# Kernel optimization log

Hardware: AMD Instinct MI355X
Metric: run time of the kernel (lower is better)

The kernel has to match this reference:

```python
import jax, jax.numpy as jnp
import numpy as np

B, S, I, H, O = 64, 512, 256, 1024, 128

def setup_inputs() -> dict:
    key = jax.random.key(0)
    ks = jax.random.split(key, 9)
    s_in = 1.0 / np.sqrt(I)
    s_h = 1.0 / np.sqrt(H)
    return {
        "x": jax.random.normal(ks[0], (B, S, I), dtype=jnp.float32),
        "W_in": jax.random.uniform(ks[1], (H, I), jnp.float32, -s_in, s_in),
        "b_in": jax.random.uniform(ks[2], (H,), jnp.float32, -s_in, s_in),
        "W_rec": jax.random.uniform(ks[3], (H, H), jnp.float32, -s_h, s_h),
        "b_rec": jax.random.uniform(ks[4], (H,), jnp.float32, -s_h, s_h),
        "tau_m": jnp.full((H,), 2.0, dtype=jnp.float32),
        "tau_n": jnp.full((H,), 2.0, dtype=jnp.float32),
        "W_out": jax.random.uniform(ks[5], (O, H), jnp.float32, -s_h, s_h),
        "b_out": jax.random.uniform(ks[6], (O,), jnp.float32, -s_h, s_h),
    }

def reference(x, W_in, b_in, W_rec, b_rec, tau_m, tau_n, W_out, b_out):
    b, s, _ = x.shape
    h = W_in.shape[0]
    alpha = jax.nn.sigmoid(tau_m)  # [H]
    beta = jax.nn.sigmoid(tau_n)   # [H]
    # Precompute feedforward GEMM for all timesteps at once: [B,S,H]
    ff = jnp.einsum('bsi,hi->bsh', x, W_in) + b_in

    def step(carry, ff_t):
        mem, d, prev_spike = carry  # each [B,H]
        total = ff_t + prev_spike @ W_rec.T + b_rec
        d = beta * d + (1.0 - beta) * total
        mem = alpha * mem + (1.0 - alpha) * d
        spike = (mem > 1.0).astype(mem.dtype)
        mem = mem * (1.0 - spike)
        out = jax.nn.sigmoid(spike @ W_out.T + b_out)  # [B,O]
        return (mem, d, spike), out

    zeros = jnp.zeros((b, h), dtype=x.dtype)
    _, outs = jax.lax.scan(step, (zeros, zeros, zeros), jnp.swapaxes(ff, 0, 1))
    return jnp.swapaxes(outs, 0, 1)  # [B,S,O]
```

## Files before the change

kernel.cpp:

```cpp
#include <hip/hip_runtime.h>
#include <hip/hip_bf16.h>
#include <stdint.h>

#define B_ 64
#define S_ 512
#define I_ 256
#define H_ 1024
#define O_ 128
#define M_ (B_*S_)

typedef float f32x4 __attribute__((ext_vector_type(4)));
typedef unsigned short u16x4 __attribute__((ext_vector_type(4)));
typedef unsigned short u16x8 __attribute__((ext_vector_type(8)));

__device__ __forceinline__ unsigned short f2bf(float f) {
    unsigned u = __float_as_uint(f);
    u += 0x7FFFu + ((u >> 16) & 1u);
    return (unsigned short)(u >> 16);
}
__device__ __forceinline__ float bf2f(unsigned short s) {
    return __uint_as_float((unsigned)s << 16);
}

__global__ void __launch_bounds__(256) k0_convert(
    const float* __restrict__ x, const float* __restrict__ Win,
    uint8_t* __restrict__ xf8, uint8_t* __restrict__ wf8,
    unsigned* __restrict__ firstCross, unsigned* __restrict__ cnt)
{
    const unsigned tid = blockIdx.x * 256 + threadIdx.x;
    const float* src;
    uint8_t* dst;
    if (tid < 524288u) {
        unsigned T = tid >> 11, rem = tid & 2047;
        unsigned kt = rem >> 10, g = (rem >> 7) & 7, r = rem & 127;
        src = x + ((size_t)(T * 128 + r)) * 256 + kt * 128 + g * 16;
        dst = xf8 + (size_t)tid * 16;
    } else {
        unsigned t2 = tid - 524288u;
        unsigned T = t2 >> 11, rem = t2 & 2047;
        unsigned kt = rem >> 10, g = (rem >> 7) & 7, r = rem & 127;
        src = Win + ((size_t)(T * 128 + r)) * 256 + kt * 128 + g * 16;
        dst = wf8 + (size_t)t2 * 16;
    }
    const float4* s4 = (const float4*)src;
    float4 a = s4[0], b = s4[1], c = s4[2], e = s4[3];
    int w0 = 0, w1 = 0, w2 = 0, w3 = 0;
    w0 = __builtin_amdgcn_cvt_pk_fp8_f32(a.x, a.y, w0, false);
    w0 = __builtin_amdgcn_cvt_pk_fp8_f32(a.z, a.w, w0, true);
    w1 = __builtin_amdgcn_cvt_pk_fp8_f32(b.x, b.y, w1, false);
    w1 = __builtin_amdgcn_cvt_pk_fp8_f32(b.z, b.w, w1, true);
    w2 = __builtin_amdgcn_cvt_pk_fp8_f32(c.x, c.y, w2, false);
    w2 = __builtin_amdgcn_cvt_pk_fp8_f32(c.z, c.w, w2, true);
    w3 = __builtin_amdgcn_cvt_pk_fp8_f32(e.x, e.y, w3, false);
    w3 = __builtin_amdgcn_cvt_pk_fp8_f32(e.z, e.w, w3, true);
    int4 o; o.x = w0; o.y = w1; o.z = w2; o.w = w3;
    *(int4*)dst = o;
    if (blockIdx.x == 0) {
        if (threadIdx.x < 64) firstCross[threadIdx.x] = 0xFFFFFFFFu;
        else if (threadIdx.x < 128) cnt[threadIdx.x - 64] = 0u;
    }
}

__global__ void __launch_bounds__(256) kf_gemm_scan(
    const uint8_t* __restrict__ xf8, const uint8_t* __restrict__ wf8,
    const float* __restrict__ b_in, const float* __restrict__ b_rec,
    const float* __restrict__ tau_m, const float* __restrict__ tau_n,
    const float* __restrict__ b_out,
    unsigned* __restrict__ firstCross, unsigned* __restrict__ cnt,
    float* __restrict__ out)
{
    __shared__ uint8_t lsbuf[32768];
    __shared__ int lastFlag;
    uint8_t* lA = lsbuf;
    uint8_t* lB = lsbuf + 16384;

    const int tid  = threadIdx.x;
    const int w    = tid >> 6;
    const int lane = tid & 63;
    const int idx  = blockIdx.x;
    const int b    = (idx & 7) | ((idx >> 6) << 3);
    const int hn   = (idx >> 3) & 7;
    const int wave_m = (w >> 1) * 64;
    const int wave_n = (w & 1) * 64;
    const int colrow = lane & 15;
    const int quad   = lane >> 4;

    float alpha = 0.f, beta = 0.f, cbr = 0.f, oma = 0.f, ombr = 0.f;
    float d = 0.f, mem = 0.f;
    unsigned cross = 0xFFFFFFFFu;
    if (tid < 128) {
        const int hs = hn * 128 + tid;
        alpha = 1.f / (1.f + expf(-tau_m[hs]));
        beta  = 1.f / (1.f + expf(-tau_n[hs]));
        oma = 1.f - alpha; ombr = 1.f - beta;
        cbr = ombr * (b_in[hs] + b_rec[hs]);
    }

    const uint8_t* gB_tile = wf8 + (size_t)hn * 32768;

    for (int tt = 0; tt < 4; ++tt) {
        const uint8_t* gA_tile = xf8 + (size_t)(b * 4 + tt) * 32768;

        f32x4 acc[4][4];
#pragma unroll
        for (int mi = 0; mi < 4; ++mi)
#pragma unroll
            for (int ni = 0; ni < 4; ++ni)
                acc[mi][ni] = (f32x4){0.f, 0.f, 0.f, 0.f};

        for (int kt = 0; kt < 2; ++kt) {
            __syncthreads();
            const int kofs = kt * 16384;
#pragma unroll
            for (int j = 0; j < 4; ++j) {
                const int chunk = ((j * 4 + w) << 10);
                __builtin_amdgcn_global_load_lds(
                    (const __attribute__((address_space(1))) void*)(gA_tile + kofs + chunk + lane * 16),
                    (__attribute__((address_space(3))) void*)(lA + chunk), 16, 0, 0);
                __builtin_amdgcn_global_load_lds(
                    (const __attribute__((address_space(1))) void*)(gB_tile + kofs + chunk + lane * 16),
                    (__attribute__((address_space(3))) void*)(lB + chunk), 16, 0, 0);
            }
            __syncthreads();

#pragma unroll
            for (int kq = 0; kq < 4; ++kq) {
                const int fo = ((kq * 2 + (quad >> 1)) << 11) + ((quad & 1) << 3);
                long long af[4], bfr[4];
#pragma unroll
                for (int i = 0; i < 4; ++i) {
                    af[i]  = *(const long long*)(lA + fo + ((wave_m + i * 16 + colrow) << 4));
                    bfr[i] = *(const long long*)(lB + fo + ((wave_n + i * 16 + colrow) << 4));
                }
#pragma unroll
                for (int mi = 0; mi < 4; ++mi)
#pragma unroll
                    for (int ni = 0; ni < 4; ++ni)
                        acc[mi][ni] = __builtin_amdgcn_mfma_f32_16x16x32_fp8_fp8(
                            af[mi], bfr[ni], acc[mi][ni], 0, 0, 0);
            }
        }
        __syncthreads();

#pragma unroll
        for (int mi = 0; mi < 4; ++mi) {
            const int t0 = wave_m + mi * 16 + quad * 4;
            const int gbase = (t0 >> 3) * 2048 + ((t0 & 4) << 1);
#pragma unroll
            for (int ni = 0; ni < 4; ++ni) {
                const int h0 = wave_n + ni * 16 + colrow;
                u16x4 p;
                p[0] = f2bf(acc[mi][ni][0]);
                p[1] = f2bf(acc[mi][ni][1]);
                p[2] = f2bf(acc[mi][ni][2]);
                p[3] = f2bf(acc[mi][ni][3]);
                *(u16x4*)(lsbuf + gbase + (h0 << 4)) = p;
            }
        }
        __syncthreads();

        if (tid < 128) {
            const uint8_t* rowp = lsbuf + tid * 16;
            for (int tl0 = 0; tl0 < 128; tl0 += 16) {
                const int gb = (tl0 >> 3) * 2048;
                u16x8 v0 = *(const u16x8*)(rowp + gb);
                u16x8 v1 = *(const u16x8*)(rowp + gb + 2048);
                float f[16];
#pragma unroll
                for (int u = 0; u < 8; ++u) { f[u] = bf2f(v0[u]); f[8 + u] = bf2f(v1[u]); }
#pragma unroll
                for (int u = 0; u < 16; ++u) {
                    d   = fmaf(beta,  d,   fmaf(ombr, f[u], cbr));
                    mem = fmaf(alpha, mem, oma * d);
                    if (mem > 1.0f) {
                        unsigned ts = (unsigned)(tt * 128 + tl0 + u);
                        if (ts < cross) cross = ts;
                    }
                }
            }
        }
    }

    if (tid < 128 && cross != 0xFFFFFFFFu) atomicMin(firstCross + b, cross);
    __syncthreads();
    if (tid == 0) {
        __threadfence();
        unsigned old = atomicAdd(cnt + b, 1u);
        int flag = 0;
        if (old == 7u) {
            __threadfence();
            unsigned fc = atomicAdd(firstCross + b, 0u);
            flag = (fc == 0xFFFFFFFFu) ? 1 : 0;
        }
        lastFlag = flag;
    }
    __syncthreads();
    if (lastFlag) {
        float* sg = (float*)lsbuf;
        if (tid < 128) sg[tid] = 1.f / (1.f + expf(-b_out[tid]));
        __syncthreads();
        const int q = tid & 31;
        float4 v = *(float4*)(sg + q * 4);
        float* obase = out + (size_t)b * (S_ * O_) + q * 4;
        const int trow = tid >> 5;
#pragma unroll 4
        for (int k = 0; k < 64; ++k)
            *(float4*)(obase + (size_t)(trow + k * 8) * O_) = v;
    }
}

__global__ void __launch_bounds__(1024) k3_repair(
    const float* __restrict__ x, const float* __restrict__ W_in,
    const float* __restrict__ b_in,
    const float* __restrict__ W_rec, const float* __restrict__ b_rec,
    const float* __restrict__ tau_m, const float* __restrict__ tau_n,
    const float* __restrict__ W_out, const float* __restrict__ b_out,
    const unsigned* __restrict__ firstCross,
    unsigned long long* __restrict__ gmask,
    float* __restrict__ out)
{
    const int b = blockIdx.x;
    if (firstCross[b] == 0xFFFFFFFFu) return;
    const int h = threadIdx.x;
    __shared__ float xrow[I_];
    __shared__ unsigned long long msk[16];
    if (h < 16) msk[h] = 0ull;
    const float alpha = 1.f / (1.f + expf(-tau_m[h]));
    const float beta  = 1.f / (1.f + expf(-tau_n[h]));
    const float bsum  = b_in[h] + b_rec[h];
    const float* wi = W_in + (size_t)h * I_;
    const float* wr = W_rec + (size_t)h * H_;
    float d = 0.f, mem = 0.f;
    for (int t = 0; t < S_; ++t) {
        __syncthreads();
        if (h < I_) xrow[h] = x[((size_t)b * S_ + t) * I_ + h];
        __syncthreads();
        float ffv = 0.f;
        for (int k = 0; k < I_; ++k) ffv += xrow[k] * wi[k];
        float rec = 0.f;
#pragma unroll
        for (int wd = 0; wd < 16; ++wd) {
            unsigned long long mw = msk[wd];
            while (mw) {
                int bit = __ffsll((long long)mw) - 1;
                rec += wr[(wd << 6) + bit];
                mw &= (mw - 1);
            }
        }
        float tot = ffv + bsum + rec;
        d   = beta  * d   + (1.f - beta)  * tot;
        mem = alpha * mem + (1.f - alpha) * d;
        int sp = (mem > 1.0f) ? 1 : 0;
        if (sp) mem = 0.f;
        unsigned long long bal = __ballot(sp);
        __syncthreads();
        if ((h & 63) == 0) {
            msk[h >> 6] = bal;
            gmask[((size_t)b * S_ + t) * 16 + (h >> 6)] = bal;
        }
    }
    __syncthreads();
    __threadfence_block();
    for (int i = h; i < S_ * O_; i += 1024) {
        const int t = i >> 7, o = i & (O_ - 1);
        float logit = b_out[o];
        const unsigned long long* m = gmask + ((size_t)b * S_ + t) * 16;
        const float* wo = W_out + (size_t)o * H_;
        for (int wd = 0; wd < 16; ++wd) {
            unsigned long long mw = m[wd];
            while (mw) {
                int bit = __ffsll((long long)mw) - 1;
                logit += wo[(wd << 6) + bit];
                mw &= (mw - 1);
            }
        }
        out[((size_t)b * S_ + t) * O_ + o] = 1.f / (1.f + expf(-logit));
    }
}

extern "C" void kernel_launch(void* const* d_in, const int* in_sizes, int n_in,
                              void* d_out, int out_size, void* d_ws, size_t ws_size,
                              hipStream_t stream) {
    const float* x     = (const float*)d_in[0];
    const float* W_in  = (const float*)d_in[1];
    const float* b_in  = (const float*)d_in[2];
    const float* W_rec = (const float*)d_in[3];
    const float* b_rec = (const float*)d_in[4];
    const float* tau_m = (const float*)d_in[5];
    const float* tau_n = (const float*)d_in[6];
    const float* W_out = (const float*)d_in[7];
    const float* b_out = (const float*)d_in[8];
    float* out = (float*)d_out;

    char* ws = (char*)d_ws;
    size_t off = 0;
    uint8_t* xf8 = (uint8_t*)(ws + off);               off += (size_t)M_ * I_;
    uint8_t* wf8 = (uint8_t*)(ws + off);               off += (size_t)H_ * I_;
    unsigned long long* gmask = (unsigned long long*)(ws + off); off += (size_t)B_ * S_ * 16 * 8;
    unsigned* firstCross = (unsigned*)(ws + off);      off += 256;
    unsigned* cnt = (unsigned*)(ws + off);             off += 256;
    if (ws_size < off) return;

    k0_convert<<<2112, 256, 0, stream>>>(x, W_in, xf8, wf8, firstCross, cnt);
    kf_gemm_scan<<<512, 256, 0, stream>>>(xf8, wf8, b_in, b_rec, tau_m, tau_n,
                                          b_out, firstCross, cnt, out);
    k3_repair<<<64, 1024, 0, stream>>>(x, W_in, b_in, W_rec, b_rec, tau_m, tau_n,
                                       W_out, b_out, firstCross, gmask, out);
}
```

Measured before the change: 138.7 us.

## Pre-swizzle FP8 operands into MFMA fragment order and load directly to registers

The conversion kernel now writes x and W_in in FP8 directly in the per-lane MFMA fragment layout. The GEMM can then read A fragments straight from global memory into registers, and the whole W_in tile per wave is preloaded into 32 registers once, skipping the LDS staging and the barriers around it. Launch bounds request 3 blocks per CU. The trade-offs are higher register pressure and dropping the LDS reuse across waves (each wave now fetches its own A fragments), while the preprocess reads become more strided.

```diff
diff --git a/kernel.cpp b/kernel.cpp
--- a/kernel.cpp
+++ b/kernel.cpp
@@ -31,19 +31,29 @@
     const float* src;
     uint8_t* dst;
     if (tid < 524288u) {
-        unsigned T = tid >> 11, rem = tid & 2047;
-        unsigned kt = rem >> 10, g = (rem >> 7) & 7, r = rem & 127;
-        src = x + ((size_t)(T * 128 + r)) * 256 + kt * 128 + g * 16;
-        dst = xf8 + (size_t)tid * 16;
+        unsigned T   = tid >> 11;
+        unsigned rem = (tid << 4) & 32767u;
+        unsigned kq  = rem >> 12;
+        unsigned rb  = (rem >> 9) & 7u;
+        unsigned l0  = (rem >> 3) & 63u;
+        src = x + ((size_t)(T * 128 + rb * 16 + (l0 & 15u))) * 256
+                + kq * 32 + (l0 >> 4) * 8;
+        dst = xf8 + ((size_t)tid << 4);
     } else {
-        unsigned t2 = tid - 524288u;
-        unsigned T = t2 >> 11, rem = t2 & 2047;
-        unsigned kt = rem >> 10, g = (rem >> 7) & 7, r = rem & 127;
-        src = Win + ((size_t)(T * 128 + r)) * 256 + kt * 128 + g * 16;
-        dst = wf8 + (size_t)t2 * 16;
-    }
-    const float4* s4 = (const float4*)src;
-    float4 a = s4[0], b = s4[1], c = s4[2], e = s4[3];
+        unsigned t2  = tid - 524288u;
+        unsigned T   = t2 >> 11;
+        unsigned rem = (t2 << 4) & 32767u;
+        unsigned kq  = rem >> 12;
+        unsigned rb  = (rem >> 9) & 7u;
+        unsigned l0  = (rem >> 3) & 63u;
+        src = Win + ((size_t)(T * 128 + rb * 16 + (l0 & 15u))) * 256
+                  + kq * 32 + (l0 >> 4) * 8;
+        dst = wf8 + ((size_t)t2 << 4);
+    }
+    float4 a = *(const float4*)src;
+    float4 b = *(const float4*)(src + 4);
+    float4 c = *(const float4*)(src + 256);
+    float4 e = *(const float4*)(src + 260);
     int w0 = 0, w1 = 0, w2 = 0, w3 = 0;
     w0 = __builtin_amdgcn_cvt_pk_fp8_f32(a.x, a.y, w0, false);
     w0 = __builtin_amdgcn_cvt_pk_fp8_f32(a.z, a.w, w0, true);
@@ -61,7 +71,7 @@
     }
 }
 
-__global__ void __launch_bounds__(256) kf_gemm_scan(
+__global__ void __launch_bounds__(256, 3) kf_gemm_scan(
     const uint8_t* __restrict__ xf8, const uint8_t* __restrict__ wf8,
     const float* __restrict__ b_in, const float* __restrict__ b_rec,
     const float* __restrict__ tau_m, const float* __restrict__ tau_n,
@@ -71,8 +81,6 @@
 {
     __shared__ uint8_t lsbuf[32768];
     __shared__ int lastFlag;
-    uint8_t* lA = lsbuf;
-    uint8_t* lB = lsbuf + 16384;
 
     const int tid  = threadIdx.x;
     const int w    = tid >> 6;
@@ -96,10 +104,17 @@
         cbr = ombr * (b_in[hs] + b_rec[hs]);
     }
 
-    const uint8_t* gB_tile = wf8 + (size_t)hn * 32768;
+    const uint8_t* wB = wf8 + (size_t)hn * 32768 + ((wave_n >> 4) << 9) + lane * 8;
+    long long bq[32];
+#pragma unroll
+    for (int kq = 0; kq < 8; ++kq)
+#pragma unroll
+        for (int ni = 0; ni < 4; ++ni)
+            bq[kq * 4 + ni] = *(const long long*)(wB + (size_t)(kq * 8 + ni) * 512);
 
     for (int tt = 0; tt < 4; ++tt) {
-        const uint8_t* gA_tile = xf8 + (size_t)(b * 4 + tt) * 32768;
+        const uint8_t* xA = xf8 + (size_t)(b * 4 + tt) * 32768
+                          + ((wave_m >> 4) << 9) + lane * 8;
 
         f32x4 acc[4][4];
 #pragma unroll
@@ -108,38 +123,20 @@
             for (int ni = 0; ni < 4; ++ni)
                 acc[mi][ni] = (f32x4){0.f, 0.f, 0.f, 0.f};
 
-        for (int kt = 0; kt < 2; ++kt) {
-            __syncthreads();
-            const int kofs = kt * 16384;
-#pragma unroll
-            for (int j = 0; j < 4; ++j) {
-                const int chunk = ((j * 4 + w) << 10);
-                __builtin_amdgcn_global_load_lds(
-                    (const __attribute__((address_space(1))) void*)(gA_tile + kofs + chunk + lane * 16),
-                    (__attribute__((address_space(3))) void*)(lA + chunk), 16, 0, 0);
-                __builtin_amdgcn_global_load_lds(
-                    (const __attribute__((address_space(1))) void*)(gB_tile + kofs + chunk + lane * 16),
-                    (__attribute__((address_space(3))) void*)(lB + chunk), 16, 0, 0);
-            }
-            __syncthreads();
-
-#pragma unroll
-            for (int kq = 0; kq < 4; ++kq) {
-                const int fo = ((kq * 2 + (quad >> 1)) << 11) + ((quad & 1) << 3);
-                long long af[4], bfr[4];
-#pragma unroll
-                for (int i = 0; i < 4; ++i) {
-                    af[i]  = *(const long long*)(lA + fo + ((wave_m + i * 16 + colrow) << 4));
-                    bfr[i] = *(const long long*)(lB + fo + ((wave_n + i * 16 + colrow) << 4));
-                }
-#pragma unroll
-                for (int mi = 0; mi < 4; ++mi)
-#pragma unroll
-                    for (int ni = 0; ni < 4; ++ni)
-                        acc[mi][ni] = __builtin_amdgcn_mfma_f32_16x16x32_fp8_fp8(
-                            af[mi], bfr[ni], acc[mi][ni], 0, 0, 0);
-            }
-        }
+#pragma unroll
+        for (int kq = 0; kq < 8; ++kq) {
+            long long a[4];
+#pragma unroll
+            for (int mi = 0; mi < 4; ++mi)
+                a[mi] = *(const long long*)(xA + (size_t)(kq * 8 + mi) * 512);
+#pragma unroll
+            for (int mi = 0; mi < 4; ++mi)
+#pragma unroll
+                for (int ni = 0; ni < 4; ++ni)
+                    acc[mi][ni] = __builtin_amdgcn_mfma_f32_16x16x32_fp8_fp8(
+                        a[mi], bq[kq * 4 + ni], acc[mi][ni], 0, 0, 0);
+        }
+
         __syncthreads();
 
 #pragma unroll
```

Measured after the change: 139.0 us. About the same (+0.2%).
